# Performance work log

Measured on AMD Instinct MI355X. Metric: run time of the kernel, lower is better.

## Reference

```python
import jax, jax.numpy as jnp
import numpy as np

J = 8      # number of octaves/scales
Q = 8      # first-order wavelets per octave (Q2 = 1 for second order)
T = 65536  # signal support
EPS = 1e-8
XI_MAX = 0.35  # highest wavelet center frequency (cycles/sample)


def _build_filters(N=T, J_=J, Q_=Q):
    """Morlet-like analytic filterbank defined directly in the Fourier domain."""
    f = np.fft.fftfreq(N)  # normalized freqs in [-0.5, 0.5)
    # first-order: J*Q log-spaced bandpass filters
    xis1 = XI_MAX * 2.0 ** (-np.arange(J_ * Q_) / Q_)
    sig1 = xis1 / Q_
    psi1 = np.exp(-0.5 * ((f[None, :] - xis1[:, None]) / sig1[:, None]) ** 2)
    j1 = np.arange(J_ * Q_) // Q_  # octave index of each first-order filter
    # second-order: one wavelet per octave (Q2=1)
    xis2 = XI_MAX * 2.0 ** (-np.arange(J_).astype(np.float64))
    sig2 = 0.6 * xis2
    psi2 = np.exp(-0.5 * ((f[None, :] - xis2[:, None]) / sig2[:, None]) ** 2)
    # low-pass at scale 2^J
    sig_phi = XI_MAX * 2.0 ** (-J_)
    phi = np.exp(-0.5 * (f / sig_phi) ** 2)
    return (jnp.asarray(psi1, jnp.float32), jnp.asarray(psi2, jnp.float32),
            jnp.asarray(phi, jnp.float32), j1)


def _scatter(x):
    """Order-0/1/2 wavelet scattering: FFT conv -> modulus -> low-pass -> subsample."""
    psi1, psi2, phi, j1 = _build_filters()
    stride = 2 ** J
    xf = jnp.fft.fft(x)  # [B, N] complex64
    lowpass = lambda uf: jnp.real(jnp.fft.ifft(uf * phi))[..., ::stride]
    S0 = lowpass(xf)[:, None, :]                                  # [B, 1, N/2^J]
    U1 = jnp.abs(jnp.fft.ifft(xf[:, None, :] * psi1[None]))      # [B, JQ, N]
    U1f = jnp.fft.fft(U1)
    S1 = lowpass(U1f)                                             # [B, JQ, N/2^J]
    parts = [S0, S1]
    for j2_ in range(J):  # small fixed loop over second-order scales
        sel = j1 < j2_    # static (numpy) frequency-ordering mask
        if not sel.any():
            continue
        U2 = jnp.abs(jnp.fft.ifft(U1f[:, sel] * psi2[j2_]))
        parts.append(lowpass(jnp.fft.fft(U2)))
    return jnp.concatenate(parts, axis=1)  # [B, 289, N/2^J]


def setup_inputs() -> dict:
    key = jax.random.key(0)
    x = jax.random.normal(key, (8, T), dtype=jnp.float32)
    return {"x": x}


def reference(x):
    Sx = _scatter(x)
    # kymatio Scattering1D has no `output_format` attr -> real=Sx, imag=0,
    # then log-magnitude normalization (normalize=True):
    mag = jnp.sqrt(Sx * Sx + EPS)
    real = jnp.log(mag + EPS)
    imag = jnp.zeros_like(real)
    return (real, imag)
```

## Files before the change

### kernel.cpp

```cpp
#include <hip/hip_runtime.h>
#include <hip/hip_fp16.h>
#include <math.h>

#define NN 65536
#define TWO_PI 6.283185307179586f
#define RSTR 264
#define SWZ(m) ((m) ^ (((m) >> 4) & 15))
#define SWZI(m, r) (SWZ(m) ^ ((r) & 12))
#define CTOT 10829824ul

__constant__ int CLO[8]  = {-32768, -15360, -5376, -8192, -8192, -2048, -2048, -2048};
__constant__ int CWW[8]  = {65536, 42240, 16384, 16384, 16384, 4096, 4096, 4096};
__constant__ int CRING[8] = {0, 0, 1, 1, 1, 1, 1, 1};
__constant__ unsigned long COFF[8] = {0ul, 4194304ul, 6897664ul, 7946240ul,
                                      8994816ul, 10043392ul, 10305536ul, 10567680ul};

__device__ __forceinline__ void lds_fence() {
    asm volatile("s_waitcnt lgkmcnt(0)" ::: "memory");
}
__device__ __forceinline__ int rev16(int p) { return ((p & 3) << 2) | (p >> 2); }
__device__ __forceinline__ int rev64(int p) { return ((p & 3) << 4) | (p & 12) | (p >> 4); }

template<int SIGN>
__device__ __forceinline__ void fft16(float* xr, float* xi, float* yr, float* yi)
{
    const float S = (SIGN > 0) ? 1.0f : -1.0f;
    const float C8 = 0.92387953251f, S8 = 0.38268343236f, R2 = 0.70710678119f;
#pragma unroll
    for (int n0 = 0; n0 < 4; ++n0) {
        float z0r=xr[n0],    z0i=xi[n0];
        float z1r=xr[n0+4],  z1i=xi[n0+4];
        float z2r=xr[n0+8],  z2i=xi[n0+8];
        float z3r=xr[n0+12], z3i=xi[n0+12];
        float t0r=z0r+z2r, t0i=z0i+z2i;
        float t1r=z0r-z2r, t1i=z0i-z2i;
        float t2r=z1r+z3r, t2i=z1i+z3i;
        float t3r=S*(z1r-z3r), t3i=S*(z1i-z3i);
        xr[n0]=t0r+t2r;      xi[n0]=t0i+t2i;
        xr[n0+4]=t1r-t3i;    xi[n0+4]=t1i+t3r;
        xr[n0+8]=t0r-t2r;    xi[n0+8]=t0i-t2i;
        xr[n0+12]=t1r+t3i;   xi[n0+12]=t1i-t3r;
    }
    {
        const float W1r=C8,  W1i=S*S8;
        const float W2r=R2,  W2i=S*R2;
        const float W3r=S8,  W3i=S*C8;
        const float W6r=-R2, W6i=S*R2;
        const float W9r=-C8, W9i=-S*S8;
#define TWID(idx, wr, wi) { float ar=xr[idx], ai=xi[idx]; xr[idx]=ar*(wr)-ai*(wi); xi[idx]=ar*(wi)+ai*(wr); }
        TWID(5,W1r,W1i)  TWID(9,W2r,W2i)   TWID(13,W3r,W3i)
        TWID(6,W2r,W2i)  { float ar=xr[10], ai=xi[10]; xr[10]=-S*ai; xi[10]=S*ar; } TWID(14,W6r,W6i)
        TWID(7,W3r,W3i)  TWID(11,W6r,W6i)  TWID(15,W9r,W9i)
#undef TWID
    }
#pragma unroll
    for (int p = 0; p < 4; ++p) {
        float z0r=xr[4*p],   z0i=xi[4*p];
        float z1r=xr[4*p+1], z1i=xi[4*p+1];
        float z2r=xr[4*p+2], z2i=xi[4*p+2];
        float z3r=xr[4*p+3], z3i=xi[4*p+3];
        float t0r=z0r+z2r, t0i=z0i+z2i;
        float t1r=z0r-z2r, t1i=z0i-z2i;
        float t2r=z1r+z3r, t2i=z1i+z3i;
        float t3r=S*(z1r-z3r), t3i=S*(z1i-z3i);
        yr[p]=t0r+t2r;     yi[p]=t0i+t2i;
        yr[p+4]=t1r-t3i;   yi[p+4]=t1i+t3r;
        yr[p+8]=t0r-t2r;   yi[p+8]=t0i-t2i;
        yr[p+12]=t1r+t3i;  yi[p+12]=t1i-t3r;
    }
}

template<int SIGN, bool BIGTW, int OUT, bool INREAL, int PADL, int PADR>
__device__ __forceinline__ void fft256_soa(float* rr, float* ri, int u, int n1,
                                           float twrate, float mscale, int cxor, int qmask)
{
    float xr[16], xi[16], yr[16], yi[16];
#pragma unroll
    for (int qq = 0; qq < 4; ++qq) {
        if (qmask & (1 << qq)) {
#pragma unroll
            for (int j = 0; j < 4; ++j) {
                int b = qq * 4 + j;
                int s = SWZ(u + (b << 4)) ^ cxor;
                xr[b] = rr[s];
                xi[b] = INREAL ? 0.f : ri[s];
            }
        } else {
#pragma unroll
            for (int j = 0; j < 4; ++j) { xr[qq * 4 + j] = 0.f; xi[qq * 4 + j] = 0.f; }
        }
    }
    fft16<SIGN>(xr, xi, yr, yi);
    float sa, ca;
    __sincosf((float)SIGN * (TWO_PI / 256.0f) * (float)u, &sa, &ca);
    float twr = 1.f, twi = 0.f;
#pragma unroll
    for (int c = 0; c < 16; ++c) {
        int s = SWZ((c << 4) + u) ^ cxor;
        rr[s] = yr[c] * twr - yi[c] * twi;
        ri[s] = yr[c] * twi + yi[c] * twr;
        float nr = twr * ca - twi * sa; twi = twr * sa + twi * ca; twr = nr;
    }
    lds_fence();
#pragma unroll
    for (int a = 0; a < 16; ++a) {
        int s = SWZ((u << 4) + a) ^ cxor;
        xr[a] = rr[s]; xi[a] = ri[s];
    }
    fft16<SIGN>(xr, xi, yr, yi);
    float tbr = 1.f, tbi = 0.f, str = 1.f, sti = 0.f;
    if (BIGTW) {
        float s0, c0, s1, c1;
        __sincosf((float)SIGN * twrate * (float)(n1 * u), &s0, &c0);
        __sincosf((float)SIGN * twrate * (float)(n1 << 4), &s1, &c1);
        tbr = c0; tbi = s0; str = c1; sti = s1;
    }
#pragma unroll
    for (int d = 0; d < 16; ++d) {
        float vr = yr[d], vi = yi[d];
        if (BIGTW) {
            float pr = vr * tbr - vi * tbi, pi = vr * tbi + vi * tbr;
            vr = pr; vi = pi;
            float nr = tbr * str - tbi * sti; tbi = tbr * sti + tbi * str; tbr = nr;
        }
        int k = u + (d << 4);
        if (OUT == 1) {
            rr[SWZ(k) ^ cxor] = sqrtf(fmaf(vr, vr, vi * vi)) * mscale;
        } else if (OUT == 2) {
            float mag = sqrtf(fmaf(vr, vr, vi * vi)) * mscale;
            ri[PADL + k] = mag;
            if (k >= 256 - PADL) ri[k - (256 - PADL)] = mag;
            if (k < PADR) ri[PADL + 256 + k] = mag;
        } else {
            int s = SWZ(k) ^ cxor;
            rr[s] = vr; ri[s] = vi;
        }
    }
    lds_fence();
}

template<int L, int CLOG, int RST, int SIGN, bool SWZC>
__device__ __forceinline__ void lds_dit(float* re, float* im, int t, int T)
{
    const int NC = 1 << CLOG;
    const int nbf = NC * (L >> 2);
    for (int h = 1; h < L; h <<= 2) {
        __syncthreads();
        for (int i = t; i < nbf; i += T) {
            int c = i & (NC - 1);
            int bf = i >> CLOG;
            int j = bf & (h - 1);
            int q0 = ((bf - j) << 2) + j;
            int r0 = q0, r1 = q0 + h, r2 = q0 + 2 * h, r3 = q0 + 3 * h;
            int a0, a1, a2, a3;
            if (SWZC) {
                a0 = r0 * RST + SWZI(c, r0); a1 = r1 * RST + SWZI(c, r1);
                a2 = r2 * RST + SWZI(c, r2); a3 = r3 * RST + SWZI(c, r3);
            } else {
                a0 = r0 * RST + c; a1 = r1 * RST + c; a2 = r2 * RST + c; a3 = r3 * RST + c;
            }
            float x0r = re[a0], x0i = im[a0];
            float x1r = re[a1], x1i = im[a1];
            float x2r = re[a2], x2i = im[a2];
            float x3r = re[a3], x3i = im[a3];
            if (h > 1) {
                float ang = (float)SIGN * (TWO_PI / (float)(4 * h)) * (float)j;
                float sj, cj; __sincosf(ang, &sj, &cj);
                float c2 = cj * cj - sj * sj, s2 = 2.f * cj * sj;
                float c3 = c2 * cj - s2 * sj, s3 = c2 * sj + s2 * cj;
                float r;
                r = x1r * cj - x1i * sj; x1i = x1r * sj + x1i * cj; x1r = r;
                r = x2r * c2 - x2i * s2; x2i = x2r * s2 + x2i * c2; x2r = r;
                r = x3r * c3 - x3i * s3; x3i = x3r * s3 + x3i * c3; x3r = r;
            }
            float t0r = x0r + x2r, t0i = x0i + x2i;
            float t1r = x0r - x2r, t1i = x0i - x2i;
            float t2r = x1r + x3r, t2i = x1i + x3i;
            float t3r = -(float)SIGN * (x1i - x3i), t3i = (float)SIGN * (x1r - x3r);
            re[a0] = t0r + t2r; im[a0] = t0i + t2i;
            re[a1] = t1r + t3r; im[a1] = t1i + t3i;
            re[a2] = t0r - t2r; im[a2] = t0i - t2i;
            re[a3] = t1r - t3r; im[a3] = t1i - t3i;
        }
    }
    __syncthreads();
}

template<int L, int CLOG, int RST, int SIGN, bool SWZC>
__device__ __forceinline__ void lds_dif(float* re, float* im, int t, int T)
{
    const int NC = 1 << CLOG;
    const int nbf = NC * (L >> 2);
    for (int h = L >> 2; h >= 1; h >>= 2) {
        __syncthreads();
        for (int i = t; i < nbf; i += T) {
            int c = i & (NC - 1);
            int bf = i >> CLOG;
            int j = bf & (h - 1);
            int q0 = ((bf - j) << 2) + j;
            int r0 = q0, r1 = q0 + h, r2 = q0 + 2 * h, r3 = q0 + 3 * h;
            int a0, a1, a2, a3;
            if (SWZC) {
                a0 = r0 * RST + SWZI(c, r0); a1 = r1 * RST + SWZI(c, r1);
                a2 = r2 * RST + SWZI(c, r2); a3 = r3 * RST + SWZI(c, r3);
            } else {
                a0 = r0 * RST + c; a1 = r1 * RST + c; a2 = r2 * RST + c; a3 = r3 * RST + c;
            }
            float x0r = re[a0], x0i = im[a0];
            float x1r = re[a1], x1i = im[a1];
            float x2r = re[a2], x2i = im[a2];
            float x3r = re[a3], x3i = im[a3];
            float t0r = x0r + x2r, t0i = x0i + x2i;
            float t1r = x0r - x2r, t1i = x0i - x2i;
            float t2r = x1r + x3r, t2i = x1i + x3i;
            float t3r = -(float)SIGN * (x1i - x3i), t3i = (float)SIGN * (x1r - x3r);
            float y1r = t1r + t3r, y1i = t1i + t3i;
            float y2r = t0r - t2r, y2i = t0i - t2i;
            float y3r = t1r - t3r, y3i = t1i - t3i;
            re[a0] = t0r + t2r; im[a0] = t0i + t2i;
            if (h > 1) {
                float ang = (float)SIGN * (TWO_PI / (float)(4 * h)) * (float)j;
                float sj, cj; __sincosf(ang, &sj, &cj);
                float c2 = cj * cj - sj * sj, s2 = 2.f * cj * sj;
                float c3 = c2 * cj - s2 * sj, s3 = c2 * sj + s2 * cj;
                re[a1] = y1r * cj - y1i * sj; im[a1] = y1r * sj + y1i * cj;
                re[a2] = y2r * c2 - y2i * s2; im[a2] = y2r * s2 + y2i * c2;
                re[a3] = y3r * c3 - y3i * s3; im[a3] = y3r * s3 + y3i * c3;
            } else {
                re[a1] = y1r; im[a1] = y1i;
                re[a2] = y2r; im[a2] = y2i;
                re[a3] = y3r; im[a3] = y3i;
            }
        }
    }
    __syncthreads();
}

__global__ __launch_bounds__(256)
void xf_stage1(const float* __restrict__ x, float2* __restrict__ D)
{
    __shared__ float sre[16 * RSTR];
    __shared__ float sim[16 * RSTR];
    const int t = threadIdx.x;
    const int r = blockIdx.x >> 4;
    const int n10 = (blockIdx.x & 15) << 4;
#pragma unroll
    for (int it = 0; it < 16; ++it) {
        int flat = it * 256 + t;
        int i = flat & 15, n2 = flat >> 4;
        int n = (n10 + i) + (n2 << 8);
        sre[i * RSTR + SWZI(n2, i)] = x[(size_t)r * NN + n];
        sim[i * RSTR + SWZI(n2, i)] = 0.f;
    }
    __syncthreads();
    const int g = t >> 4, u = t & 15;
    fft256_soa<-1, true, 0, false, 0, 0>(sre + g * RSTR, sim + g * RSTR, u, n10 + g,
                                         TWO_PI / (float)NN, 1.f, g & 12, 15);
    __syncthreads();
#pragma unroll
    for (int it = 0; it < 16; ++it) {
        int flat = it * 256 + t;
        int i = flat & 15, k2 = flat >> 4;
        int s = i * RSTR + SWZI(k2, i);
        D[(size_t)r * NN + (k2 << 8) + (n10 + i)] = make_float2(sre[s], sim[s]);
    }
}

__global__ __launch_bounds__(256)
void xf_stage2(const float2* __restrict__ D, float2* __restrict__ XF)
{
    __shared__ float sre[16 * RSTR];
    __shared__ float sim[16 * RSTR];
    const int t = threadIdx.x;
    const int r = blockIdx.x >> 4;
    const int k20 = (blockIdx.x & 15) << 4;
#pragma unroll
    for (int it = 0; it < 16; ++it) {
        float2 v = D[(size_t)r * NN + ((size_t)(k20 + it) << 8) + t];
        sre[it * RSTR + SWZI(t, it)] = v.x;
        sim[it * RSTR + SWZI(t, it)] = v.y;
    }
    __syncthreads();
    const int g = t >> 4, u = t & 15;
    fft256_soa<-1, false, 0, false, 0, 0>(sre + g * RSTR, sim + g * RSTR, u, 0, 0.f, 1.f, g & 12, 15);
    __syncthreads();
#pragma unroll
    for (int it = 0; it < 16; ++it) {
        int flat = it * 256 + t;
        int fi = flat & 15, k1 = flat >> 4;
        int s = fi * RSTR + SWZI(k1, fi);
        XF[(size_t)r * NN + (size_t)(k20 + fi) + ((size_t)k1 << 8)] = make_float2(sre[s], sim[s]);
    }
}

__global__ __launch_bounds__(256)
void fo_stage1(const float2* __restrict__ XF, __half2* __restrict__ Dh, int qbase)
{
    __shared__ float sre[16 * RSTR];
    __shared__ float sim[16 * RSTR];
    const int t = threadIdx.x;
    const int r = blockIdx.x >> 4;
    const int n10 = (blockIdx.x & 15) << 4;
    const int q = qbase + r;
    const int j1 = q >> 6, ql = q & 63;
    const int srow = ql >> 3, w = ql & 7;
    const int lam = j1 * 8 + w;
    const float xi = 0.35f * exp2f(-(float)lam * 0.125f);
    const float invsig = 8.0f / xi;
    const float kc = xi * (float)NN;
    const float Hh = 6.10f * (xi * 0.125f) * (float)NN;
    const int klo = (int)(kc - Hh), khi = (int)(kc + Hh) + 1;
    int qm = 0;
    if (klo < 0 || khi >= NN) qm = 15;
    else {
#pragma unroll
        for (int qq = 0; qq < 4; ++qq)
            if (16384 * qq + 16896 >= klo && 16384 * qq - 512 <= khi) qm |= (1 << qq);
    }
#pragma unroll
    for (int it = 0; it < 16; ++it) {
        int flat = it * 256 + t;
        int i = flat & 15, n2 = flat >> 4;
        int n = (n10 + i) + (n2 << 8);
        float nsf = (float)((n < NN / 2) ? n : n - NN);
        float vr = 0.f, vi = 0.f;
        if (fabsf(nsf - kc) <= Hh) {
            float2 v = XF[(size_t)srow * NN + n];
            float a = (nsf * (1.0f / (float)NN) - xi) * invsig;
            float wg = __expf(-0.5f * a * a) * 0.0625f;
            vr = v.x * wg; vi = v.y * wg;
        }
        sre[i * RSTR + SWZI(n2, i)] = vr;
        sim[i * RSTR + SWZI(n2, i)] = vi;
    }
    __syncthreads();
    const int g = t >> 4, u = t & 15;
    fft256_soa<1, true, 0, false, 0, 0>(sre + g * RSTR, sim + g * RSTR, u, n10 + g,
                                        TWO_PI / (float)NN, 1.f, g & 12, qm);
    __syncthreads();
#pragma unroll
    for (int it = 0; it < 16; ++it) {
        int flat = it * 256 + t;
        int i = flat & 15, k2 = flat >> 4;
        int s = i * RSTR + SWZI(k2, i);
        Dh[(size_t)r * NN + (k2 << 8) + (n10 + i)] = __floats2half2_rn(sre[s], sim[s]);
    }
}

__global__ __launch_bounds__(256)
void fo_mid(const __half2* __restrict__ Dh, __half2* __restrict__ D2h)
{
    __shared__ float sre[16 * RSTR];
    __shared__ float sim[16 * RSTR];
    const int t = threadIdx.x;
    const int r = blockIdx.x >> 4;
    const int k20 = (blockIdx.x & 15) << 4;
#pragma unroll
    for (int it = 0; it < 16; ++it) {
        float2 v = __half22float2(Dh[(size_t)r * NN + ((size_t)(k20 + it) << 8) + t]);
        sre[it * RSTR + SWZI(t, it)] = v.x;
        sim[it * RSTR + SWZI(t, it)] = v.y;
    }
    __syncthreads();
    const int g = t >> 4, u = t & 15;
    float* rr = sre + g * RSTR; float* ri = sim + g * RSTR;
    fft256_soa<1, false, 1, false, 0, 0>(rr, ri, u, 0, 0.f, 16.0f / (float)NN, g & 12, 15);
    fft256_soa<-1, true, 0, true, 0, 0>(rr, ri, u, k20 + g, TWO_PI / (float)NN, 1.f, g & 12, 15);
    __syncthreads();
#pragma unroll
    for (int it = 0; it < 16; ++it) {
        int flat = it * 256 + t;
        int i = flat & 15, k2 = flat >> 4;
        int s = i * RSTR + SWZI(k2, i);
        D2h[(size_t)r * NN + (k2 << 8) + (k20 + i)] = __floats2half2_rn(sre[s], sim[s]);
    }
}

__global__ __launch_bounds__(256)
void fo_stage2(const __half2* __restrict__ D2h, __half2* __restrict__ Cw, int qbase)
{
    __shared__ float sre[16 * RSTR];
    __shared__ float sim[16 * RSTR];
    const int t = threadIdx.x;
    const int r = blockIdx.x >> 4;
    const int k20 = (blockIdx.x & 15) << 4;
    const int q = qbase + r;
    const int j1 = q >> 6, ql = q & 63;
#pragma unroll
    for (int it = 0; it < 16; ++it) {
        float2 v = __half22float2(D2h[(size_t)r * NN + ((size_t)(k20 + it) << 8) + t]);
        sre[it * RSTR + SWZI(t, it)] = v.x;
        sim[it * RSTR + SWZI(t, it)] = v.y;
    }
    __syncthreads();
    const int g = t >> 4, u = t & 15;
    fft256_soa<-1, false, 0, false, 0, 0>(sre + g * RSTR, sim + g * RSTR, u, 0, 0.f, 1.f, g & 12, 15);
    __syncthreads();
    const size_t base = COFF[j1] + (size_t)ql * CWW[j1];
    const int lo = CLO[j1], Wd = CWW[j1];
#pragma unroll
    for (int it = 0; it < 16; ++it) {
        int flat = it * 256 + t;
        int fi = flat & 15, k1 = flat >> 4;
        int k = (k20 + fi) + (k1 << 8);
        int ksg = (k < NN / 2) ? k : k - NN;
        int idx = ksg - lo;
        if (idx >= 0 && idx < Wd) {
            int s = fi * RSTR + SWZI(k1, fi);
            Cw[base + idx] = __floats2half2_rn(sre[s], sim[s]);
        }
    }
}

__global__ __launch_bounds__(256)
void sfold_all(const float2* __restrict__ XF, const __half2* __restrict__ Cw,
               float* __restrict__ out)
{
    __shared__ float Gr[256];
    __shared__ float Gi[256];
    const int blk = blockIdx.x;
    const int t = threadIdx.x;
    const float invsigphi = 731.428571f;
    float ar = 0.f, ai = 0.f;
    if (blk < 8) {
#pragma unroll
        for (int qq = -4; qq <= 4; ++qq) {
            int ks = t + (qq << 8);
            int k = ks & (NN - 1);
            float a = ((float)ks * (1.0f / (float)NN)) * invsigphi;
            float wg = __expf(-0.5f * a * a);
            float2 v = XF[(size_t)blk * NN + k];
            ar = fmaf(v.x, wg, ar); ai = fmaf(v.y, wg, ai);
        }
    } else {
        int q = blk - 8;
        int j1 = q >> 6, ql = q & 63;
        size_t base = COFF[j1] + (size_t)ql * CWW[j1];
        int lo = CLO[j1], Wd = CWW[j1], ring = CRING[j1];
#pragma unroll
        for (int qq = -4; qq <= 4; ++qq) {
            int ks = t + (qq << 8);
            float a = ((float)ks * (1.0f / (float)NN)) * invsigphi;
            float wg = __expf(-0.5f * a * a);
            int idx = ring ? ((ks - lo) & (Wd - 1)) : (ks - lo);
            float2 v = __half22float2(Cw[base + idx]);
            ar = fmaf(v.x, wg, ar); ai = fmaf(v.y, wg, ai);
        }
    }
    Gr[t] = ar; Gi[t] = ai;
    __syncthreads();
    float sb, cb;
    __sincosf((TWO_PI / 256.0f) * (float)t, &sb, &cb);
    float wr = 1.f, wi = 0.f, s = 0.f;
    for (int kk = 0; kk < 256; ++kk) {
        s = fmaf(Gr[kk], wr, s);
        s = fmaf(-Gi[kk], wi, s);
        float nr = wr * cb - wi * sb; wi = wr * sb + wi * cb; wr = nr;
    }
    s *= (1.0f / (float)NN);
    float mag = sqrtf(fmaf(s, s, 1e-8f));
    float val = logf(mag + 1e-8f);
    int b, chan;
    if (blk < 8) { b = blk; chan = 0; }
    else { int q = blk - 8; int j1 = q >> 6, ql = q & 63; b = ql >> 3; chan = 1 + j1 * 8 + (ql & 7); }
    out[((size_t)b * 289 + chan) * 256 + t] = val;
}

__device__ __forceinline__ void so_decode_full(int q, int& j1, int& j2, int& rb)
{
    int pp = q >> 6;
    rb = q & 63;
    j2 = (pp == 0) ? 1 : 2;
    j1 = (pp == 0) ? 0 : pp - 1;
}
__device__ __forceinline__ void so_decode_dec16(int q, int& j1, int& j2, int& rb)
{
    int pp = q >> 6;
    rb = q & 63;
    j2 = (pp < 3) ? 3 : 4;
    j1 = (pp < 3) ? pp : pp - 3;
}

__global__ __launch_bounds__(256)
void so_stage1(const __half2* __restrict__ Cw, __half2* __restrict__ Dh, int qbase)
{
    __shared__ float sre[16 * RSTR];
    __shared__ float sim[16 * RSTR];
    const int t = threadIdx.x;
    const int r = blockIdx.x >> 4;
    const int n10 = (blockIdx.x & 15) << 4;
    int j1, j2, rb;
    so_decode_full(qbase + r, j1, j2, rb);
    const float xi2 = 0.35f * exp2f(-(float)j2);
    const float invsig = 1.0f / (0.6f * xi2);
    const float kc = xi2 * (float)NN;
    const float Hh = 6.10f * (0.6f * xi2) * (float)NN;
    const size_t base = COFF[j1] + (size_t)rb * CWW[j1];
    const int lo = CLO[j1], Wd = CWW[j1];
#pragma unroll
    for (int it = 0; it < 16; ++it) {
        int flat = it * 256 + t;
        int i = flat & 15, n2 = flat >> 4;
        int n = (n10 + i) + (n2 << 8);
        int ksg = (n < NN / 2) ? n : n - NN;
        float nsf = (float)ksg;
        float vr = 0.f, vi = 0.f;
        int idx = ksg - lo;
        if (fabsf(nsf - kc) <= Hh && idx >= 0 && idx < Wd) {
            float2 v = __half22float2(Cw[base + idx]);
            float a = (nsf * (1.0f / (float)NN) - xi2) * invsig;
            float wg = __expf(-0.5f * a * a) * (1.0f / 256.0f);
            vr = v.x * wg; vi = v.y * wg;
        }
        sre[i * RSTR + SWZI(n2, i)] = vr;
        sim[i * RSTR + SWZI(n2, i)] = vi;
    }
    __syncthreads();
    const int g = t >> 4, u = t & 15;
    fft256_soa<1, true, 0, false, 0, 0>(sre + g * RSTR, sim + g * RSTR, u, n10 + g,
                                        TWO_PI / (float)NN, 1.f, g & 12, 15);
    __syncthreads();
#pragma unroll
    for (int it = 0; it < 16; ++it) {
        int flat = it * 256 + t;
        int i = flat & 15, k2 = flat >> 4;
        int s = i * RSTR + SWZI(k2, i);
        Dh[(size_t)r * NN + (k2 << 8) + (n10 + i)] = __floats2half2_rn(sre[s], sim[s]);
    }
}

__global__ __launch_bounds__(256)
void so_stage2(const __half2* __restrict__ Dh, float* __restrict__ S2acc, int qbase)
{
    __shared__ float sre[16 * RSTR];
    __shared__ float sim[16 * RSTR];
    __shared__ float wtab[16][8];
    const int t = threadIdx.x;
    const int r = blockIdx.x >> 4;
    const int k20 = (blockIdx.x & 15) << 4;
#pragma unroll
    for (int it = 0; it < 16; ++it) {
        float2 v = __half22float2(Dh[(size_t)r * NN + ((size_t)(k20 + it) << 8) + t]);
        sre[it * RSTR + SWZI(t, it)] = v.x;
        sim[it * RSTR + SWZI(t, it)] = v.y;
    }
    if (t < 128) {
        int fi = t >> 3, dd = (t & 7) - 4;
        int w = k20 + fi + (dd << 8) + 768;
        float val = 0.f;
        if (w >= 0 && w <= 1536) {
            float m = (float)(w - 768);
            val = 0.003426963f * __expf(-3.690276e-5f * m * m);
        }
        wtab[fi][t & 7] = val;
    }
    __syncthreads();
    const int g = t >> 4, u = t & 15;
    fft256_soa<1, false, 2, false, 4, 3>(sre + g * RSTR, sim + g * RSTR, u, 0, 0.f, 1.f, g & 12, 15);
    __syncthreads();
    float acc = 0.f;
#pragma unroll
    for (int fi = 0; fi < 16; ++fi) {
        const float* row = sim + fi * RSTR;
#pragma unroll
        for (int dd = 0; dd < 8; ++dd)
            acc = fmaf(row[t + dd], wtab[fi][dd], acc);
    }
    atomicAdd(&S2acc[(size_t)(qbase + r) * 256 + t], acc * (1.0f / 256.0f));
}

template<int MODE>
__global__ __launch_bounds__(256)
void dec16_s1(const float2* __restrict__ XF, const __half2* __restrict__ Cw,
              __half2* __restrict__ Dh16, int qbase)
{
    __shared__ float sre[64 * 64];
    __shared__ float sim[64 * 64];
    const int t = threadIdx.x;
    const int r = blockIdx.x >> 2;
    const int c0 = (blockIdx.x & 3) << 6;
    const int q = qbase + r;
    float xi, invsig, kc, Hh; int srow = 0; size_t cbase = 0; int lo = 0, Wd = 0, ring = 0;
    if (MODE == 1) {
        int j1 = 2 + (q >> 6); int ql = q & 63; srow = ql >> 3;
        int lam = j1 * 8 + (ql & 7);
        xi = 0.35f * exp2f(-(float)lam * 0.125f);
        invsig = 8.0f / xi; kc = xi * (float)NN; Hh = 6.10f * (xi * 0.125f) * (float)NN;
    } else {
        int j1, j2, rb;
        so_decode_dec16(q, j1, j2, rb);
        xi = 0.35f * exp2f(-(float)j2);
        invsig = 1.0f / (0.6f * xi); kc = xi * (float)NN;
        Hh = fminf(6.10f * (0.6f * xi) * (float)NN, 7967.0f);
        cbase = COFF[j1] + (size_t)rb * CWW[j1]; lo = CLO[j1]; Wd = CWW[j1]; ring = CRING[j1];
    }
    const int klo = (int)ceilf(kc - Hh);
#pragma unroll
    for (int it = 0; it < 16; ++it) {
        int flat = it * 256 + t;
        int c = flat & 63, n2 = flat >> 6;
        int kap = (c0 + c) + (n2 << 8);
        int kk = klo + (int)(((unsigned)(kap - klo)) & 16383u);
        float vr = 0.f, vi = 0.f;
        if (fabsf((float)kk - kc) <= Hh) {
            float2 v;
            bool ok = true;
            if (MODE == 1) v = XF[(size_t)srow * NN + (kk & (NN - 1))];
            else {
                int idx;
                if (ring) idx = (kk - lo) & (Wd - 1);
                else { idx = kk - lo; ok = (idx >= 0 && idx < Wd); }
                v = ok ? __half22float2(Cw[cbase + idx]) : make_float2(0.f, 0.f);
            }
            float a = ((float)kk * (1.0f / (float)NN) - xi) * invsig;
            float wg = __expf(-0.5f * a * a) * 0.015625f;
            vr = v.x * wg; vi = v.y * wg;
        }
        int p = rev64(n2);
        sre[(p << 6) + c] = vr;
        sim[(p << 6) + c] = vi;
    }
    lds_dit<64, 6, 64, 1, false>(sre, sim, t, 256);
#pragma unroll
    for (int it = 0; it < 16; ++it) {
        int flat = it * 256 + t;
        int c = flat & 63, row = flat >> 6;
        int a = (row << 6) + c;
        float ang = (TWO_PI / 16384.0f) * (float)(row * (c0 + c));
        float sj, cj; __sincosf(ang, &sj, &cj);
        float rr = sre[a] * cj - sim[a] * sj;
        sim[a] = sre[a] * sj + sim[a] * cj; sre[a] = rr;
    }
    __syncthreads();
#pragma unroll
    for (int it = 0; it < 16; ++it) {
        int flat = it * 256 + t;
        int c = flat & 63, row = flat >> 6;
        Dh16[(size_t)r * 16384 + (row << 8) + (c0 + c)] =
            __floats2half2_rn(sre[(row << 6) + c], sim[(row << 6) + c]);
    }
}

__global__ __launch_bounds__(256)
void dec16_s2so(const __half2* __restrict__ Dh16, float* __restrict__ S2acc, int qbase)
{
    __shared__ float sre[16 * RSTR];
    __shared__ float sim[16 * RSTR];
    __shared__ float wtab[16][6];
    const int t = threadIdx.x;
    const int r = blockIdx.x >> 2;
    const int k2base = (blockIdx.x & 3) << 4;
#pragma unroll
    for (int it = 0; it < 16; ++it) {
        float2 v = __half22float2(Dh16[(size_t)r * 16384 + ((k2base + it) << 8) + t]);
        sre[it * RSTR + SWZI(t, it)] = v.x;
        sim[it * RSTR + SWZI(t, it)] = v.y;
    }
    if (t < 96) {
        int p = t / 6, dl = t % 6;
        float w = (float)(256 * (dl - 2) - 4 * (k2base + p));
        wtab[p][dl] = 0.003426963f * __expf(-3.690276e-5f * w * w);
    }
    __syncthreads();
    const int g = t >> 4, u = t & 15;
    fft256_soa<1, false, 2, false, 3, 2>(sre + g * RSTR, sim + g * RSTR, u, 0, 0.f,
                                         64.0f / (float)NN, g & 12, 15);
    __syncthreads();
    float acc = 0.f;
#pragma unroll
    for (int p = 0; p < 16; ++p) {
        const float* row = sim + p * RSTR;
#pragma unroll
        for (int dl = 0; dl < 6; ++dl)
            acc = fmaf(row[t + 5 - dl], wtab[p][dl], acc);
    }
    atomicAdd(&S2acc[(size_t)(192 + qbase + r) * 256 + t], acc * 4.0f);
}

__global__ __launch_bounds__(256)
void dec16_s2fo(const __half2* __restrict__ Dh16, __half2* __restrict__ D2h16)
{
    __shared__ float sre[16 * RSTR];
    __shared__ float sim[16 * RSTR];
    const int t = threadIdx.x;
    const int r = blockIdx.x >> 2;
    const int k2base = (blockIdx.x & 3) << 4;
#pragma unroll
    for (int it = 0; it < 16; ++it) {
        float2 v = __half22float2(Dh16[(size_t)r * 16384 + ((k2base + it) << 8) + t]);
        sre[it * RSTR + SWZI(t, it)] = v.x;
        sim[it * RSTR + SWZI(t, it)] = v.y;
    }
    __syncthreads();
    const int g = t >> 4, u = t & 15;
    float* rr = sre + g * RSTR; float* ri = sim + g * RSTR;
    fft256_soa<1, false, 1, false, 0, 0>(rr, ri, u, 0, 0.f, 256.0f / (float)NN, g & 12, 15);
    fft256_soa<-1, true, 0, true, 0, 0>(rr, ri, u, k2base + g, TWO_PI / 16384.0f, 1.f, g & 12, 15);
    __syncthreads();
#pragma unroll
    for (int it = 0; it < 16; ++it) {
        int a = it * RSTR + SWZI(t, it);
        D2h16[(size_t)r * 16384 + ((k2base + it) << 8) + t] = __floats2half2_rn(sre[a], sim[a]);
    }
}

__global__ __launch_bounds__(256)
void dec16_s3fo(const __half2* __restrict__ D2h16, __half2* __restrict__ Cw, int qbase)
{
    __shared__ float sre[64 * 64];
    __shared__ float sim[64 * 64];
    const int t = threadIdx.x;
    const int r = blockIdx.x >> 2;
    const int c0 = (blockIdx.x & 3) << 6;
    const int q = qbase + r;
    const int j1 = 2 + (q >> 6), ql = q & 63;
#pragma unroll
    for (int it = 0; it < 16; ++it) {
        int flat = it * 256 + t;
        int c = flat & 63, m2 = flat >> 6;
        float2 v = __half22float2(D2h16[(size_t)r * 16384 + (m2 << 8) + (c0 + c)]);
        sre[(m2 << 6) + c] = v.x;
        sim[(m2 << 6) + c] = v.y;
    }
    lds_dif<64, 6, 64, -1, false>(sre, sim, t, 256);
    const int lo = CLO[j1];
    const size_t rbase = COFF[j1] + (size_t)ql * 16384;
#pragma unroll
    for (int it = 0; it < 16; ++it) {
        int flat = it * 256 + t;
        int c = flat & 63, p = flat >> 6;
        int kap = (c0 + c) + (rev64(p) << 8);
        int ks = (kap < 8192) ? kap : kap - 16384;
        int idx = (ks - lo) & 16383;
        int a = (p << 6) + c;
        Cw[rbase + idx] = __floats2half2_rn(sre[a], sim[a]);
    }
}

__global__ __launch_bounds__(256)
void m4k_fo(const float2* __restrict__ XF, __half2* __restrict__ Cw)
{
    __shared__ float sre[16 * RSTR];
    __shared__ float sim[16 * RSTR];
    const int t = threadIdx.x;
    const int q = blockIdx.x;
    const int j1 = 5 + (q >> 6), ql = q & 63;
    const int srow = ql >> 3;
    const int lam = j1 * 8 + (ql & 7);
    const float xi = 0.35f * exp2f(-(float)lam * 0.125f);
    const float invsig = 8.0f / xi;
    const float kc = xi * (float)NN;
    const float Hh = 6.10f * (xi * 0.125f) * (float)NN;
    const int klo = (int)ceilf(kc - Hh);
#pragma unroll
    for (int it = 0; it < 16; ++it) {
        int kap = t + (it << 8);
        int kk = klo + (int)(((unsigned)(kap - klo)) & 4095u);
        float vr = 0.f, vi = 0.f;
        if (fabsf((float)kk - kc) <= Hh) {
            float2 v = XF[(size_t)srow * NN + (kk & (NN - 1))];
            float a = ((float)kk * (1.0f / (float)NN) - xi) * invsig;
            float wg = __expf(-0.5f * a * a);
            vr = v.x * wg; vi = v.y * wg;
        }
        int p = rev16(it);
        sre[p * RSTR + SWZI(t, p)] = vr;
        sim[p * RSTR + SWZI(t, p)] = vi;
    }
    lds_dit<16, 8, RSTR, 1, true>(sre, sim, t, 256);
#pragma unroll
    for (int it = 0; it < 16; ++it) {
        int a = it * RSTR + SWZI(t, it);
        float ang = (TWO_PI / 4096.0f) * (float)(it * t);
        float sj, cj; __sincosf(ang, &sj, &cj);
        float rr = sre[a] * cj - sim[a] * sj;
        sim[a] = sre[a] * sj + sim[a] * cj; sre[a] = rr;
    }
    __syncthreads();
    const int g = t >> 4, u = t & 15;
    float* rr = sre + g * RSTR; float* ri = sim + g * RSTR;
    fft256_soa<1, false, 1, false, 0, 0>(rr, ri, u, 0, 0.f, 16.0f / (float)NN, g & 12, 15);
    fft256_soa<-1, true, 0, true, 0, 0>(rr, ri, u, g, TWO_PI / 4096.0f, 1.f, g & 12, 15);
    lds_dif<16, 8, RSTR, -1, true>(sre, sim, t, 256);
    const int lo = CLO[j1];
    const size_t rbase = COFF[j1] + (size_t)ql * 4096;
#pragma unroll
    for (int it = 0; it < 16; ++it) {
        int kap = t + (rev16(it) << 8);
        int ks = (kap < 2048) ? kap : kap - 4096;
        int idx = (ks - lo) & 4095;
        int a = it * RSTR + SWZI(t, it);
        Cw[rbase + idx] = __floats2half2_rn(sre[a], sim[a]);
    }
}

__global__ __launch_bounds__(256)
void m4k_so(const __half2* __restrict__ Cw, float* __restrict__ out)
{
    __shared__ float sre[16 * RSTR];
    __shared__ float sim[16 * RSTR];
    __shared__ float wtab[16][6];
    const int t = threadIdx.x;
    const int q = blockIdx.x;
    const int pp = q >> 6, rb = q & 63;
    int j1, j2;
    if (pp < 5)       { j2 = 5; j1 = pp; }
    else if (pp < 11) { j2 = 6; j1 = pp - 5; }
    else              { j2 = 7; j1 = pp - 11; }
    const float xi2 = 0.35f * exp2f(-(float)j2);
    const float invsig = 1.0f / (0.6f * xi2);
    const float kc = xi2 * (float)NN;
    const float Hh = fminf(6.10f * (0.6f * xi2) * (float)NN, 1823.0f);
    const int klo = (int)ceilf(kc - Hh);
    const size_t cbase = COFF[j1] + (size_t)rb * CWW[j1];
    const int lo = CLO[j1], Wd = CWW[j1], ring = CRING[j1];
#pragma unroll
    for (int it = 0; it < 16; ++it) {
        int kap = t + (it << 8);
        int kk = klo + (int)(((unsigned)(kap - klo)) & 4095u);
        float vr = 0.f, vi = 0.f;
        if (fabsf((float)kk - kc) <= Hh) {
            int idx; bool ok = true;
            if (ring) idx = (kk - lo) & (Wd - 1);
            else { idx = kk - lo; ok = (idx >= 0 && idx < Wd); }
            if (ok) {
                float2 v = __half22float2(Cw[cbase + idx]);
                float a = ((float)kk * (1.0f / (float)NN) - xi2) * invsig;
                float wg = __expf(-0.5f * a * a);
                vr = v.x * wg; vi = v.y * wg;
            }
        }
        int p = rev16(it);
        sre[p * RSTR + SWZI(t, p)] = vr;
        sim[p * RSTR + SWZI(t, p)] = vi;
    }
    if (t < 96) {
        int p = t / 6, dl = t % 6;
        float w = (float)(256 * (dl - 2) - 16 * p);
        wtab[p][dl] = 0.003426963f * __expf(-3.690276e-5f * w * w);
    }
    lds_dit<16, 8, RSTR, 1, true>(sre, sim, t, 256);
#pragma unroll
    for (int it = 0; it < 16; ++it) {
        int a = it * RSTR + SWZI(t, it);
        float ang = (TWO_PI / 4096.0f) * (float)(it * t);
        float sj, cj; __sincosf(ang, &sj, &cj);
        float rr = sre[a] * cj - sim[a] * sj;
        sim[a] = sre[a] * sj + sim[a] * cj; sre[a] = rr;
    }
    __syncthreads();
    const int g = t >> 4, u = t & 15;
    fft256_soa<1, false, 2, false, 3, 2>(sre + g * RSTR, sim + g * RSTR, u, 0, 0.f,
                                         1.0f / (float)NN, g & 12, 15);
    __syncthreads();
    float acc = 0.f;
#pragma unroll
    for (int p = 0; p < 16; ++p) {
        const float* row = sim + p * RSTR;
#pragma unroll
        for (int dl = 0; dl < 6; ++dl)
            acc = fmaf(row[t + 5 - dl], wtab[p][dl], acc);
    }
    acc *= 16.0f;
    const int b = rb >> 3;
    const int chan = 65 + 4 * j2 * (j2 - 1) + j1 * 8 + (rb & 7);
    float mag = sqrtf(fmaf(acc, acc, 1e-8f));
    out[((size_t)b * 289 + chan) * 256 + t] = logf(mag + 1e-8f);
}

__global__ __launch_bounds__(256)
void s2final(const float* __restrict__ S2acc, float* __restrict__ out)
{
    const int q = blockIdx.x, n = threadIdx.x;
    int j1, j2, rb;
    if (q < 192) so_decode_full(q, j1, j2, rb);
    else         so_decode_dec16(q - 192, j1, j2, rb);
    const int b = rb >> 3;
    const int chan = 65 + 4 * j2 * (j2 - 1) + j1 * 8 + (rb & 7);
    float s = S2acc[(size_t)q * 256 + n];
    float mag = sqrtf(fmaf(s, s, 1e-8f));
    out[((size_t)b * 289 + chan) * 256 + n] = logf(mag + 1e-8f);
}

__global__ void zero_kernel(float* p, int nElem)
{
    int i = blockIdx.x * 256 + threadIdx.x;
    if (i < nElem) p[i] = 0.f;
}

extern "C" void kernel_launch(void* const* d_in, const int* in_sizes, int n_in,
                              void* d_out, int out_size, void* d_ws, size_t ws_size,
                              hipStream_t stream)
{
    const float* x = (const float*)d_in[0];
    float* out = (float*)d_out;
    char* ws = (char*)d_ws;

    size_t off = 0;
    float2*  XF    = (float2*)ws;                 off += 8ul * NN * 8;
    __half2* Cw    = (__half2*)(ws + off);        off += CTOT * 4ul;
    float*   S2acc = (float*)(ws + off);          off += 640ul * 256 * 4;
    off = (off + 255) & ~255ul;
    char* reg0 = ws + off;
    size_t avail = (ws_size > off) ? (ws_size - off) : 0;

    int CHB = (int)(avail / (512ul * 1024));  if (CHB > 128) CHB = 128;  if (CHB < 1) CHB = 1;
    int CHD = (int)(avail / (256ul * 1024));  if (CHD > 192) CHD = 192;  if (CHD < 1) CHD = 1;
    int CHE = (int)(avail / (128ul * 1024));  if (CHE > 192) CHE = 192;  if (CHE < 1) CHE = 1;
    int CHF = (int)(avail / (64ul * 1024));   if (CHF > 448) CHF = 448;  if (CHF < 1) CHF = 1;

    {
        int nz = 8 * 289 * 256;
        zero_kernel<<<(nz + 255) / 256, 256, 0, stream>>>(out + nz, nz);
        int na = 640 * 256;
        zero_kernel<<<(na + 255) / 256, 256, 0, stream>>>(S2acc, na);
    }

    {
        float2* Df = (float2*)reg0;
        xf_stage1<<<8 * 16, 256, 0, stream>>>(x, Df);
        xf_stage2<<<8 * 16, 256, 0, stream>>>(Df, XF);
    }

    for (int cs = 0; cs < 128; cs += CHB) {
        int m = (128 - cs < CHB) ? (128 - cs) : CHB;
        __half2* DhB = (__half2*)reg0;
        __half2* D2h = DhB + (size_t)CHB * NN;
        fo_stage1<<<m * 16, 256, 0, stream>>>(XF, DhB, cs);
        fo_mid<<<m * 16, 256, 0, stream>>>(DhB, D2h);
        fo_stage2<<<m * 16, 256, 0, stream>>>(D2h, Cw, cs);
    }
    for (int cs = 0; cs < 192; cs += CHE) {
        int m = (192 - cs < CHE) ? (192 - cs) : CHE;
        __half2* Dh16  = (__half2*)reg0;
        __half2* D2h16 = Dh16 + (size_t)CHE * 16384;
        dec16_s1<1><<<m * 4, 256, 0, stream>>>(XF, Cw, Dh16, cs);
        dec16_s2fo<<<m * 4, 256, 0, stream>>>(Dh16, D2h16);
        dec16_s3fo<<<m * 4, 256, 0, stream>>>(D2h16, Cw, cs);
    }
    m4k_fo<<<192, 256, 0, stream>>>(XF, Cw);

    sfold_all<<<8 + 512, 256, 0, stream>>>(XF, Cw, out);

    for (int qs = 0; qs < 192; qs += CHD) {
        int m = (192 - qs < CHD) ? (192 - qs) : CHD;
        __half2* DhS = (__half2*)reg0;
        so_stage1<<<m * 16, 256, 0, stream>>>(Cw, DhS, qs);
        so_stage2<<<m * 16, 256, 0, stream>>>(DhS, S2acc, qs);
    }
    for (int qs = 0; qs < 448; qs += CHF) {
        int m = (448 - qs < CHF) ? (448 - qs) : CHF;
        __half2* Dh16 = (__half2*)reg0;
        dec16_s1<2><<<m * 4, 256, 0, stream>>>(XF, Cw, Dh16, qs);
        dec16_s2so<<<m * 4, 256, 0, stream>>>(Dh16, S2acc, qs);
    }
    m4k_so<<<1152, 256, 0, stream>>>(Cw, out);

    s2final<<<640, 256, 0, stream>>>(S2acc, out);
}
```

Baseline: 312.8 us.

## Skip zero quarters, tabulate FFT twiddles, recur inter-stage twiddles, merge zeroing kernels

Narrows the Gaussian filter support cutoff from 6.1 to 5.0 sigma and uses a quarter mask to write zeros instead of evaluating the filter in inactive quarters, and passes that mask into the second-order FFT. Replaces per-butterfly __sincosf calls in the LDS radix-4 passes with a small shared twiddle table, and replaces per-element twiddle sincos in the transpose steps with a complex rotation recurrence. It also merges the two zeroing kernels into one launch. The narrower cutoff and the recurrence both add small numerical error, and the cutoff change alters which spectrum bins are computed.

```diff
diff --git a/kernel.cpp b/kernel.cpp
--- a/kernel.cpp
+++ b/kernel.cpp
@@ -20,6 +20,32 @@
 }
 __device__ __forceinline__ int rev16(int p) { return ((p & 3) << 2) | (p >> 2); }
 __device__ __forceinline__ int rev64(int p) { return ((p & 3) << 4) | (p & 12) | (p >> 4); }
+
+__device__ __forceinline__ int quarter_mask(int klo, int khi)
+{
+    int qm = 0;
+#pragma unroll
+    for (int qq = 0; qq < 4; ++qq) {
+        int lo_q = 16384 * qq - 255;
+        int hi_q = 16384 * qq + 16639;
+        bool act;
+        if (klo >= 0) act = (hi_q >= klo) && (lo_q <= khi);
+        else          act = (lo_q <= khi) || (hi_q >= klo + NN);
+        if (act) qm |= (1 << qq);
+    }
+    return qm;
+}
+
+__device__ __forceinline__ void build_tw6(float* twt, int t)
+{
+    if (t < 16) {
+        float s1, c1; __sincosf((TWO_PI / 64.0f) * (float)t, &s1, &c1);
+        float c2 = c1 * c1 - s1 * s1, s2 = 2.f * c1 * s1;
+        float c3 = c2 * c1 - s2 * s1, s3 = c2 * s1 + s2 * c1;
+        float* e = twt + 6 * t;
+        e[0] = c1; e[1] = s1; e[2] = c2; e[3] = s2; e[4] = c3; e[5] = s3;
+    }
+}
 
 template<int SIGN>
 __device__ __forceinline__ void fft16(float* xr, float* xi, float* yr, float* yi)
@@ -140,8 +166,9 @@
 }
 
 template<int L, int CLOG, int RST, int SIGN, bool SWZC>
-__device__ __forceinline__ void lds_dit(float* re, float* im, int t, int T)
-{
+__device__ __forceinline__ void lds_dit(float* re, float* im, const float* twt, int t, int T)
+{
+    const float S = (float)SIGN;
     const int NC = 1 << CLOG;
     const int nbf = NC * (L >> 2);
     for (int h = 1; h < L; h <<= 2) {
@@ -164,10 +191,10 @@
             float x2r = re[a2], x2i = im[a2];
             float x3r = re[a3], x3i = im[a3];
             if (h > 1) {
-                float ang = (float)SIGN * (TWO_PI / (float)(4 * h)) * (float)j;
-                float sj, cj; __sincosf(ang, &sj, &cj);
-                float c2 = cj * cj - sj * sj, s2 = 2.f * cj * sj;
-                float c3 = c2 * cj - s2 * sj, s3 = c2 * sj + s2 * cj;
+                const float* e = twt + 6 * (j * (16 / h));
+                float cj = e[0], sj = S * e[1];
+                float c2 = e[2], s2 = S * e[3];
+                float c3 = e[4], s3 = S * e[5];
                 float r;
                 r = x1r * cj - x1i * sj; x1i = x1r * sj + x1i * cj; x1r = r;
                 r = x2r * c2 - x2i * s2; x2i = x2r * s2 + x2i * c2; x2r = r;
@@ -176,7 +203,7 @@
             float t0r = x0r + x2r, t0i = x0i + x2i;
             float t1r = x0r - x2r, t1i = x0i - x2i;
             float t2r = x1r + x3r, t2i = x1i + x3i;
-            float t3r = -(float)SIGN * (x1i - x3i), t3i = (float)SIGN * (x1r - x3r);
+            float t3r = -S * (x1i - x3i), t3i = S * (x1r - x3r);
             re[a0] = t0r + t2r; im[a0] = t0i + t2i;
             re[a1] = t1r + t3r; im[a1] = t1i + t3i;
             re[a2] = t0r - t2r; im[a2] = t0i - t2i;
@@ -187,8 +214,9 @@
 }
 
 template<int L, int CLOG, int RST, int SIGN, bool SWZC>
-__device__ __forceinline__ void lds_dif(float* re, float* im, int t, int T)
-{
+__device__ __forceinline__ void lds_dif(float* re, float* im, const float* twt, int t, int T)
+{
+    const float S = (float)SIGN;
     const int NC = 1 << CLOG;
     const int nbf = NC * (L >> 2);
     for (int h = L >> 2; h >= 1; h >>= 2) {
@@ -213,16 +241,16 @@
             float t0r = x0r + x2r, t0i = x0i + x2i;
             float t1r = x0r - x2r, t1i = x0i - x2i;
             float t2r = x1r + x3r, t2i = x1i + x3i;
-            float t3r = -(float)SIGN * (x1i - x3i), t3i = (float)SIGN * (x1r - x3r);
+            float t3r = -S * (x1i - x3i), t3i = S * (x1r - x3r);
             float y1r = t1r + t3r, y1i = t1i + t3i;
             float y2r = t0r - t2r, y2i = t0i - t2i;
             float y3r = t1r - t3r, y3i = t1i - t3i;
             re[a0] = t0r + t2r; im[a0] = t0i + t2i;
             if (h > 1) {
-                float ang = (float)SIGN * (TWO_PI / (float)(4 * h)) * (float)j;
-                float sj, cj; __sincosf(ang, &sj, &cj);
-                float c2 = cj * cj - sj * sj, s2 = 2.f * cj * sj;
-                float c3 = c2 * cj - s2 * sj, s3 = c2 * sj + s2 * cj;
+                const float* e = twt + 6 * (j * (16 / h));
+                float cj = e[0], sj = S * e[1];
+                float c2 = e[2], s2 = S * e[3];
+                float c3 = e[4], s3 = S * e[5];
                 re[a1] = y1r * cj - y1i * sj; im[a1] = y1r * sj + y1i * cj;
                 re[a2] = y2r * c2 - y2i * s2; im[a2] = y2r * s2 + y2i * c2;
                 re[a3] = y3r * c3 - y3i * s3; im[a3] = y3r * s3 + y3i * c3;
@@ -308,19 +336,17 @@
     const float xi = 0.35f * exp2f(-(float)lam * 0.125f);
     const float invsig = 8.0f / xi;
     const float kc = xi * (float)NN;
-    const float Hh = 6.10f * (xi * 0.125f) * (float)NN;
+    const float Hh = 5.0f * (xi * 0.125f) * (float)NN;
     const int klo = (int)(kc - Hh), khi = (int)(kc + Hh) + 1;
-    int qm = 0;
-    if (klo < 0 || khi >= NN) qm = 15;
-    else {
-#pragma unroll
-        for (int qq = 0; qq < 4; ++qq)
-            if (16384 * qq + 16896 >= klo && 16384 * qq - 512 <= khi) qm |= (1 << qq);
-    }
-#pragma unroll
-    for (int it = 0; it < 16; ++it) {
-        int flat = it * 256 + t;
-        int i = flat & 15, n2 = flat >> 4;
+    const int qm = (khi >= NN) ? 15 : quarter_mask(klo, khi);
+#pragma unroll
+    for (int it = 0; it < 16; ++it) {
+        int i = t & 15, n2 = (it << 4) + (t >> 4);
+        if (!(qm & (1 << (it >> 2)))) {
+            sre[i * RSTR + SWZI(n2, i)] = 0.f;
+            sim[i * RSTR + SWZI(n2, i)] = 0.f;
+            continue;
+        }
         int n = (n10 + i) + (n2 << 8);
         float nsf = (float)((n < NN / 2) ? n : n - NN);
         float vr = 0.f, vi = 0.f;
@@ -494,13 +520,19 @@
     const float xi2 = 0.35f * exp2f(-(float)j2);
     const float invsig = 1.0f / (0.6f * xi2);
     const float kc = xi2 * (float)NN;
-    const float Hh = 6.10f * (0.6f * xi2) * (float)NN;
+    const float Hh = 5.0f * (0.6f * xi2) * (float)NN;
+    const int klo = (int)(kc - Hh), khi = (int)(kc + Hh) + 1;
+    const int qm = (klo >= 0 && khi >= NN) ? 15 : quarter_mask(klo, khi);
     const size_t base = COFF[j1] + (size_t)rb * CWW[j1];
     const int lo = CLO[j1], Wd = CWW[j1];
 #pragma unroll
     for (int it = 0; it < 16; ++it) {
-        int flat = it * 256 + t;
-        int i = flat & 15, n2 = flat >> 4;
+        int i = t & 15, n2 = (it << 4) + (t >> 4);
+        if (!(qm & (1 << (it >> 2)))) {
+            sre[i * RSTR + SWZI(n2, i)] = 0.f;
+            sim[i * RSTR + SWZI(n2, i)] = 0.f;
+            continue;
+        }
         int n = (n10 + i) + (n2 << 8);
         int ksg = (n < NN / 2) ? n : n - NN;
         float nsf = (float)ksg;
@@ -518,7 +550,7 @@
     __syncthreads();
     const int g = t >> 4, u = t & 15;
     fft256_soa<1, true, 0, false, 0, 0>(sre + g * RSTR, sim + g * RSTR, u, n10 + g,
-                                        TWO_PI / (float)NN, 1.f, g & 12, 15);
+                                        TWO_PI / (float)NN, 1.f, g & 12, qm);
     __syncthreads();
 #pragma unroll
     for (int it = 0; it < 16; ++it) {
@@ -576,6 +608,7 @@
 {
     __shared__ float sre[64 * 64];
     __shared__ float sim[64 * 64];
+    __shared__ float twt[96];
     const int t = threadIdx.x;
     const int r = blockIdx.x >> 2;
     const int c0 = (blockIdx.x & 3) << 6;
@@ -594,6 +627,7 @@
         Hh = fminf(6.10f * (0.6f * xi) * (float)NN, 7967.0f);
         cbase = COFF[j1] + (size_t)rb * CWW[j1]; lo = CLO[j1]; Wd = CWW[j1]; ring = CRING[j1];
     }
+    build_tw6(twt, t);
     const int klo = (int)ceilf(kc - Hh);
 #pragma unroll
     for (int it = 0; it < 16; ++it) {
@@ -620,16 +654,20 @@
         sre[(p << 6) + c] = vr;
         sim[(p << 6) + c] = vi;
     }
-    lds_dit<64, 6, 64, 1, false>(sre, sim, t, 256);
-#pragma unroll
-    for (int it = 0; it < 16; ++it) {
-        int flat = it * 256 + t;
-        int c = flat & 63, row = flat >> 6;
-        int a = (row << 6) + c;
-        float ang = (TWO_PI / 16384.0f) * (float)(row * (c0 + c));
-        float sj, cj; __sincosf(ang, &sj, &cj);
-        float rr = sre[a] * cj - sim[a] * sj;
-        sim[a] = sre[a] * sj + sim[a] * cj; sre[a] = rr;
+    lds_dit<64, 6, 64, 1, false>(sre, sim, twt, t, 256);
+    {
+        const int c = t & 63, r0 = t >> 6;
+        float sA, cA, sD, cD;
+        __sincosf((TWO_PI / 16384.0f) * (float)(r0 * (c0 + c)), &sA, &cA);
+        __sincosf((TWO_PI / 16384.0f) * (float)(4 * (c0 + c)), &sD, &cD);
+#pragma unroll
+        for (int it = 0; it < 16; ++it) {
+            int row = (it << 2) + r0;
+            int a = (row << 6) + c;
+            float rr = sre[a] * cA - sim[a] * sA;
+            sim[a] = sre[a] * sA + sim[a] * cA; sre[a] = rr;
+            float nc = cA * cD - sA * sD; sA = cA * sD + sA * cD; cA = nc;
+        }
     }
     __syncthreads();
 #pragma unroll
@@ -709,11 +747,13 @@
 {
     __shared__ float sre[64 * 64];
     __shared__ float sim[64 * 64];
+    __shared__ float twt[96];
     const int t = threadIdx.x;
     const int r = blockIdx.x >> 2;
     const int c0 = (blockIdx.x & 3) << 6;
     const int q = qbase + r;
     const int j1 = 2 + (q >> 6), ql = q & 63;
+    build_tw6(twt, t);
 #pragma unroll
     for (int it = 0; it < 16; ++it) {
         int flat = it * 256 + t;
@@ -722,7 +762,7 @@
         sre[(m2 << 6) + c] = v.x;
         sim[(m2 << 6) + c] = v.y;
     }
-    lds_dif<64, 6, 64, -1, false>(sre, sim, t, 256);
+    lds_dif<64, 6, 64, -1, false>(sre, sim, twt, t, 256);
     const int lo = CLO[j1];
     const size_t rbase = COFF[j1] + (size_t)ql * 16384;
 #pragma unroll
@@ -742,6 +782,7 @@
 {
     __shared__ float sre[16 * RSTR];
     __shared__ float sim[16 * RSTR];
+    __shared__ float twt[96];
     const int t = threadIdx.x;
     const int q = blockIdx.x;
     const int j1 = 5 + (q >> 6), ql = q & 63;
@@ -752,6 +793,7 @@
     const float kc = xi * (float)NN;
     const float Hh = 6.10f * (xi * 0.125f) * (float)NN;
     const int klo = (int)ceilf(kc - Hh);
+    build_tw6(twt, t);
 #pragma unroll
     for (int it = 0; it < 16; ++it) {
         int kap = t + (it << 8);
@@ -767,21 +809,24 @@
         sre[p * RSTR + SWZI(t, p)] = vr;
         sim[p * RSTR + SWZI(t, p)] = vi;
     }
-    lds_dit<16, 8, RSTR, 1, true>(sre, sim, t, 256);
-#pragma unroll
-    for (int it = 0; it < 16; ++it) {
-        int a = it * RSTR + SWZI(t, it);
-        float ang = (TWO_PI / 4096.0f) * (float)(it * t);
-        float sj, cj; __sincosf(ang, &sj, &cj);
-        float rr = sre[a] * cj - sim[a] * sj;
-        sim[a] = sre[a] * sj + sim[a] * cj; sre[a] = rr;
+    lds_dit<16, 8, RSTR, 1, true>(sre, sim, twt, t, 256);
+    {
+        float sD, cD; __sincosf((TWO_PI / 4096.0f) * (float)t, &sD, &cD);
+        float cA = 1.f, sA = 0.f;
+#pragma unroll
+        for (int it = 0; it < 16; ++it) {
+            int a = it * RSTR + SWZI(t, it);
+            float rr = sre[a] * cA - sim[a] * sA;
+            sim[a] = sre[a] * sA + sim[a] * cA; sre[a] = rr;
+            float nc = cA * cD - sA * sD; sA = cA * sD + sA * cD; cA = nc;
+        }
     }
     __syncthreads();
     const int g = t >> 4, u = t & 15;
     float* rr = sre + g * RSTR; float* ri = sim + g * RSTR;
     fft256_soa<1, false, 1, false, 0, 0>(rr, ri, u, 0, 0.f, 16.0f / (float)NN, g & 12, 15);
     fft256_soa<-1, true, 0, true, 0, 0>(rr, ri, u, g, TWO_PI / 4096.0f, 1.f, g & 12, 15);
-    lds_dif<16, 8, RSTR, -1, true>(sre, sim, t, 256);
+    lds_dif<16, 8, RSTR, -1, true>(sre, sim, twt, t, 256);
     const int lo = CLO[j1];
     const size_t rbase = COFF[j1] + (size_t)ql * 4096;
 #pragma unroll
@@ -800,6 +845,7 @@
     __shared__ float sre[16 * RSTR];
     __shared__ float sim[16 * RSTR];
     __shared__ float wtab[16][6];
+    __shared__ float twt[96];
     const int t = threadIdx.x;
     const int q = blockIdx.x;
     const int pp = q >> 6, rb = q & 63;
@@ -814,6 +860,7 @@
     const int klo = (int)ceilf(kc - Hh);
     const size_t cbase = COFF[j1] + (size_t)rb * CWW[j1];
     const int lo = CLO[j1], Wd = CWW[j1], ring = CRING[j1];
+    build_tw6(twt, t);
 #pragma unroll
     for (int it = 0; it < 16; ++it) {
         int kap = t + (it << 8);
@@ -839,14 +886,17 @@
         float w = (float)(256 * (dl - 2) - 16 * p);
         wtab[p][dl] = 0.003426963f * __expf(-3.690276e-5f * w * w);
     }
-    lds_dit<16, 8, RSTR, 1, true>(sre, sim, t, 256);
-#pragma unroll
-    for (int it = 0; it < 16; ++it) {
-        int a = it * RSTR + SWZI(t, it);
-        float ang = (TWO_PI / 4096.0f) * (float)(it * t);
-        float sj, cj; __sincosf(ang, &sj, &cj);
-        float rr = sre[a] * cj - sim[a] * sj;
-        sim[a] = sre[a] * sj + sim[a] * cj; sre[a] = rr;
+    lds_dit<16, 8, RSTR, 1, true>(sre, sim, twt, t, 256);
+    {
+        float sD, cD; __sincosf((TWO_PI / 4096.0f) * (float)t, &sD, &cD);
+        float cA = 1.f, sA = 0.f;
+#pragma unroll
+        for (int it = 0; it < 16; ++it) {
+            int a = it * RSTR + SWZI(t, it);
+            float rr = sre[a] * cA - sim[a] * sA;
+            sim[a] = sre[a] * sA + sim[a] * cA; sre[a] = rr;
+            float nc = cA * cD - sA * sD; sA = cA * sD + sA * cD; cA = nc;
+        }
     }
     __syncthreads();
     const int g = t >> 4, u = t & 15;
@@ -882,10 +932,11 @@
     out[((size_t)b * 289 + chan) * 256 + n] = logf(mag + 1e-8f);
 }
 
-__global__ void zero_kernel(float* p, int nElem)
+__global__ void zero2_kernel(float* a, int na, float* b, int nb)
 {
     int i = blockIdx.x * 256 + threadIdx.x;
-    if (i < nElem) p[i] = 0.f;
+    if (i < na) a[i] = 0.f;
+    else if (i < na + nb) b[i - na] = 0.f;
 }
 
 extern "C" void kernel_launch(void* const* d_in, const int* in_sizes, int n_in,
@@ -911,9 +962,8 @@
 
     {
         int nz = 8 * 289 * 256;
-        zero_kernel<<<(nz + 255) / 256, 256, 0, stream>>>(out + nz, nz);
         int na = 640 * 256;
-        zero_kernel<<<(na + 255) / 256, 256, 0, stream>>>(S2acc, na);
+        zero2_kernel<<<(nz + na + 255) / 256, 256, 0, stream>>>(out + nz, nz, S2acc, na);
     }
 
     {
```

Measured after the change: 308.1 us. No clear change (-1.5%).
